# Kernel optimization log

Hardware: AMD Instinct MI355X
Metric: run time of the kernel (lower is better)

## Reference

```python
import jax, jax.numpy as jnp
import numpy as np

DIM = 1024

def setup_inputs() -> dict:
    key = jax.random.key(0)
    ks = jax.random.split(key, 6)
    B, T, D = 8, 2048, DIM
    s = 1.0 / np.sqrt(D)
    x = jax.random.normal(ks[0], (B, T, D), dtype=jnp.float32)
    Wq = jax.random.normal(ks[1], (D, D), dtype=jnp.float32) * s
    Wk = jax.random.normal(ks[2], (D, D), dtype=jnp.float32) * s
    Wv = jax.random.normal(ks[3], (D, D), dtype=jnp.float32) * s
    Wp = jax.random.normal(ks[4], (D, D), dtype=jnp.float32) * s
    bp = jax.random.normal(ks[5], (D,), dtype=jnp.float32) * 0.01
    return {"x": x, "Wq": Wq, "Wk": Wk, "Wv": Wv, "Wp": Wp, "bp": bp}

def reference(x, Wq, Wk, Wv, Wp, bp):
    # x: [b, t, d]; weights stored as [d_in, d_out] (torch Linear applies x @ W.T;
    # here we bake the transpose into the stored matrix).
    scale = x.shape[-1] ** (-0.5)
    q = jnp.einsum('btd,de->bte', x, Wq)
    k = jnp.einsum('btd,de->bte', x, Wk)
    v = jnp.einsum('btd,de->bte', x, Wv)
    attn = jax.nn.softmax(jnp.einsum('btd,bTd->btT', q, k) * scale, axis=-1)
    out = jnp.einsum('btT,bTd->btd', attn, v)
    return jnp.einsum('btd,de->bte', out, Wp) + bp
```

## Files before the change

### kernel.cpp

```cpp
#include <hip/hip_runtime.h>


typedef _Float16 half_t;
typedef _Float16 half8 __attribute__((ext_vector_type(8)));
typedef float floatx4 __attribute__((ext_vector_type(4)));

#define GLD16(gp, lp)                                                          \
    __builtin_amdgcn_global_load_lds(                                          \
        (const __attribute__((address_space(1))) void*)(gp),                   \
        (__attribute__((address_space(3))) void*)(lp), 16, 0, 0)

template<bool OUTF32, bool TSTORE, bool BIAS>
__global__ __launch_bounds__(256, 2)
void gemm16(const half_t* __restrict__ A, const half_t* __restrict__ B,
            void* __restrict__ Cv, const float* __restrict__ bias,
            int K, int lda, int ldb, int ldc,
            long long bsA, long long bsB, long long bsC, float alpha)
{
    __shared__ half_t As[128 * 32];
    __shared__ half_t Bs[128 * 32];

    const int tid  = threadIdx.x;
    const int lane = tid & 63;
    const int wid  = tid >> 6;
    const int wr   = (wid >> 1) * 64;
    const int wc   = (wid & 1) * 64;
    const long long z = blockIdx.z;
    const int rowBase = blockIdx.y * 128;
    const int colBase = blockIdx.x * 128;

    const int srow = wid * 32 + (lane >> 2);
    const int scol = (lane & 3) * 8;

    const half_t* ga0 = A + z * bsA + (long long)(rowBase + srow) * lda + scol;
    const half_t* ga1 = ga0 + 16LL * lda;
    const half_t* gb0 = B + z * bsB + (long long)(colBase + srow) * ldb + scol;
    const half_t* gb1 = gb0 + 16LL * ldb;
    half_t* la0 = &As[(wid * 32) * 32];
    half_t* la1 = &As[(wid * 32 + 16) * 32];
    half_t* lb0 = &Bs[(wid * 32) * 32];
    half_t* lb1 = &Bs[(wid * 32 + 16) * 32];

    floatx4 acc[4][4];
    #pragma unroll
    for (int m = 0; m < 4; ++m)
        #pragma unroll
        for (int n = 0; n < 4; ++n)
            #pragma unroll
            for (int j = 0; j < 4; ++j) acc[m][n][j] = 0.0f;

    const int fr = lane & 15;
    const int fk = (lane >> 4) * 8;

    for (int kk = 0; kk < K; kk += 32) {
        __syncthreads();
        GLD16(ga0 + kk, la0);
        GLD16(ga1 + kk, la1);
        GLD16(gb0 + kk, lb0);
        GLD16(gb1 + kk, lb1);
        __syncthreads();

        half8 af[4], bf[4];
        #pragma unroll
        for (int m = 0; m < 4; ++m)
            af[m] = *(const half8*)&As[(wr + m * 16 + fr) * 32 + fk];
        #pragma unroll
        for (int n = 0; n < 4; ++n)
            bf[n] = *(const half8*)&Bs[(wc + n * 16 + fr) * 32 + fk];
        #pragma unroll
        for (int m = 0; m < 4; ++m)
            #pragma unroll
            for (int n = 0; n < 4; ++n)
                acc[m][n] = __builtin_amdgcn_mfma_f32_16x16x32_f16(af[m], bf[n], acc[m][n], 0, 0, 0);
    }

    const int ecol = lane & 15;
    const int q4   = (lane >> 4) * 4;
    #pragma unroll
    for (int m = 0; m < 4; ++m) {
        #pragma unroll
        for (int n = 0; n < 4; ++n) {
            const int gcol = colBase + wc + n * 16 + ecol;
            #pragma unroll
            for (int r = 0; r < 4; ++r) {
                const int grow = rowBase + wr + m * 16 + q4 + r;
                float v = acc[m][n][r] * alpha;
                if (BIAS) v += bias[gcol];
                if (TSTORE) {
                    const long long bb = grow >> 11;
                    const long long tt = grow & 2047;
                    ((half_t*)Cv)[bb * bsC + (long long)gcol * ldc + tt] = (half_t)v;
                } else {
                    const long long idx = z * bsC + (long long)grow * ldc + gcol;
                    if (OUTF32) ((float*)Cv)[idx] = v;
                    else        ((half_t*)Cv)[idx] = (half_t)v;
                }
            }
        }
    }
}

__global__ __launch_bounds__(256)
void cast16(const float* __restrict__ x, half_t* __restrict__ y)
{
    const long long i = ((long long)blockIdx.x * 256 + threadIdx.x) * 8;
    floatx4 a = *(const floatx4*)(x + i);
    floatx4 b = *(const floatx4*)(x + i + 4);
    half8 h;
    #pragma unroll
    for (int j = 0; j < 4; ++j) { h[j] = (half_t)a[j]; h[j + 4] = (half_t)b[j]; }
    *(half8*)(y + i) = h;
}

__global__ __launch_bounds__(256)
void cast_transpose(const float* __restrict__ W, half_t* __restrict__ WT)
{
    __shared__ float t[32][33];
    const int bx = blockIdx.x * 32, by = blockIdx.y * 32;
    const int tx = threadIdx.x, ty = threadIdx.y;
    #pragma unroll
    for (int i = 0; i < 32; i += 8)
        t[ty + i][tx] = W[(long long)(by + ty + i) * 1024 + bx + tx];
    __syncthreads();
    #pragma unroll
    for (int i = 0; i < 32; i += 8)
        WT[(long long)(bx + ty + i) * 1024 + by + tx] = (half_t)t[tx][ty + i];
}

__global__ __launch_bounds__(256)
void softmax_rows(const float* __restrict__ S, half_t* __restrict__ P)
{
    const long long base = (long long)blockIdx.x * 2048;
    const int t = threadIdx.x;
    float v[8];
    #pragma unroll
    for (int i = 0; i < 8; ++i) v[i] = S[base + i * 256 + t];
    float m = -3.0e38f;
    #pragma unroll
    for (int i = 0; i < 8; ++i) m = fmaxf(m, v[i]);
    #pragma unroll
    for (int off = 32; off > 0; off >>= 1) m = fmaxf(m, __shfl_down(m, off));
    __shared__ float redm[4], reds[4];
    const int lane = t & 63, wid = t >> 6;
    if (lane == 0) redm[wid] = m;
    __syncthreads();
    const float M = fmaxf(fmaxf(redm[0], redm[1]), fmaxf(redm[2], redm[3]));
    float s = 0.f;
    #pragma unroll
    for (int i = 0; i < 8; ++i) { v[i] = __expf(v[i] - M); s += v[i]; }
    #pragma unroll
    for (int off = 32; off > 0; off >>= 1) s += __shfl_down(s, off);
    if (lane == 0) reds[wid] = s;
    __syncthreads();
    const float inv = 1.0f / (reds[0] + reds[1] + reds[2] + reds[3]);
    #pragma unroll
    for (int i = 0; i < 8; ++i) P[base + i * 256 + t] = (half_t)(v[i] * inv);
}

extern "C" void kernel_launch(void* const* d_in, const int* in_sizes, int n_in,
                              void* d_out, int out_size, void* d_ws, size_t ws_size,
                              hipStream_t stream)
{
    const float* x  = (const float*)d_in[0];
    const float* Wq = (const float*)d_in[1];
    const float* Wk = (const float*)d_in[2];
    const float* Wv = (const float*)d_in[3];
    const float* Wp = (const float*)d_in[4];
    const float* bp = (const float*)d_in[5];
    float* out = (float*)d_out;

    char* ws = (char*)d_ws;
    const long long MB = 1024LL * 1024LL;
    half_t* WqT = (half_t*)(ws + 0 * MB);
    half_t* WkT = (half_t*)(ws + 2 * MB);
    half_t* WvT = (half_t*)(ws + 4 * MB);
    half_t* WpT = (half_t*)(ws + 6 * MB);
    half_t* q   = (half_t*)(ws + 8 * MB);
    half_t* k   = (half_t*)(ws + 40 * MB);
    half_t* vT  = (half_t*)(ws + 72 * MB);
    half_t* x16 = (half_t*)(ws + 104 * MB);

    const int ZB = (ws_size >= (size_t)(200 * MB)) ? 4
                 : (ws_size >= (size_t)(152 * MB)) ? 2 : 1;
    float*  S = (float*)(ws + 104 * MB);
    half_t* P = (half_t*)(ws + (104 + ZB * 16) * MB);

    dim3 blk(256);
    cast16<<<8192, blk, 0, stream>>>(x, x16);
    dim3 tb(32, 8), tg(32, 32);
    cast_transpose<<<tg, tb, 0, stream>>>(Wq, WqT);
    cast_transpose<<<tg, tb, 0, stream>>>(Wk, WkT);
    cast_transpose<<<tg, tb, 0, stream>>>(Wv, WvT);
    cast_transpose<<<tg, tb, 0, stream>>>(Wp, WpT);

    gemm16<false, false, false><<<dim3(8, 128, 1), blk, 0, stream>>>(
        x16, WqT, q, nullptr, 1024, 1024, 1024, 1024, 0, 0, 0, 0.03125f);
    gemm16<false, false, false><<<dim3(8, 128, 1), blk, 0, stream>>>(
        x16, WkT, k, nullptr, 1024, 1024, 1024, 1024, 0, 0, 0, 1.0f);
    gemm16<false, true,  false><<<dim3(8, 128, 1), blk, 0, stream>>>(
        x16, WvT, vT, nullptr, 1024, 1024, 1024, 2048, 0, 0, 2048LL * 1024, 1.0f);

    for (int g = 0; g < 8 / ZB; ++g) {
        const long long off = (long long)g * ZB * 2048 * 1024;
        half_t* qp = q  + off;
        half_t* kp = k  + off;
        half_t* vp = vT + off;
        half_t* cp = q  + off;

        gemm16<true, false, false><<<dim3(16, 16, ZB), blk, 0, stream>>>(
            qp, kp, S, nullptr, 1024, 1024, 1024, 2048,
            2048LL * 1024, 2048LL * 1024, 2048LL * 2048, 1.0f);
        softmax_rows<<<ZB * 2048, blk, 0, stream>>>(S, P);
        gemm16<false, false, false><<<dim3(8, 16, ZB), blk, 0, stream>>>(
            P, vp, cp, nullptr, 2048, 2048, 2048, 1024,
            2048LL * 2048, 1024LL * 2048, 2048LL * 1024, 1.0f);
    }

    gemm16<true, false, true><<<dim3(8, 128, 1), blk, 0, stream>>>(
        q, WpT, out, bp, 1024, 1024, 1024, 1024, 0, 0, 0, 1.0f);
}
```

Baseline: 561.7 us.

## Fuse QKV projections, batch all attention heads, store scores in fp16 in place

```diff
diff --git a/kernel.cpp b/kernel.cpp
--- a/kernel.cpp
+++ b/kernel.cpp
@@ -10,12 +10,12 @@
         (const __attribute__((address_space(1))) void*)(gp),                   \
         (__attribute__((address_space(3))) void*)(lp), 16, 0, 0)
 
-template<bool OUTF32, bool TSTORE, bool BIAS>
+template<int EPI>
 __global__ __launch_bounds__(256, 2)
 void gemm16(const half_t* __restrict__ A, const half_t* __restrict__ B,
-            void* __restrict__ Cv, const float* __restrict__ bias,
-            int K, int lda, int ldb, int ldc,
-            long long bsA, long long bsB, long long bsC, float alpha)
+            void* __restrict__ Cv, void* __restrict__ C2, void* __restrict__ C3,
+            const float* __restrict__ bias, int K, int lda, int ldb, int ldc,
+            long long bsA, long long bsB, long long bsC)
 {
     __shared__ half_t As[128 * 32];
     __shared__ half_t Bs[128 * 32];
@@ -84,16 +84,23 @@
             #pragma unroll
             for (int r = 0; r < 4; ++r) {
                 const int grow = rowBase + wr + m * 16 + q4 + r;
-                float v = acc[m][n][r] * alpha;
-                if (BIAS) v += bias[gcol];
-                if (TSTORE) {
-                    const long long bb = grow >> 11;
-                    const long long tt = grow & 2047;
-                    ((half_t*)Cv)[bb * bsC + (long long)gcol * ldc + tt] = (half_t)v;
+                float v = acc[m][n][r];
+                if (EPI == 0) {
+                    ((half_t*)Cv)[z * bsC + (long long)grow * ldc + gcol] = (half_t)v;
+                } else if (EPI == 1) {
+                    ((float*)Cv)[(long long)grow * ldc + gcol] = v + bias[gcol];
                 } else {
-                    const long long idx = z * bsC + (long long)grow * ldc + gcol;
-                    if (OUTF32) ((float*)Cv)[idx] = v;
-                    else        ((half_t*)Cv)[idx] = (half_t)v;
+                    const int mat = colBase >> 10;
+                    const int c   = gcol & 1023;
+                    if (mat == 0) {
+                        ((half_t*)Cv)[(long long)grow * 1024 + c] = (half_t)(v * 0.03125f);
+                    } else if (mat == 1) {
+                        ((half_t*)C2)[(long long)grow * 1024 + c] = (half_t)v;
+                    } else {
+                        const long long bb = grow >> 11;
+                        const long long tt = grow & 2047;
+                        ((half_t*)C3)[bb * (1024LL * 2048) + (long long)c * 2048 + tt] = (half_t)v;
+                    }
                 }
             }
         }
@@ -113,8 +120,13 @@
 }
 
 __global__ __launch_bounds__(256)
-void cast_transpose(const float* __restrict__ W, half_t* __restrict__ WT)
-{
+void cast_transpose4(const float* __restrict__ W0, const float* __restrict__ W1,
+                     const float* __restrict__ W2, const float* __restrict__ W3,
+                     half_t* __restrict__ WT)
+{
+    const float* W = (blockIdx.z == 0) ? W0 : (blockIdx.z == 1) ? W1
+                   : (blockIdx.z == 2) ? W2 : W3;
+    half_t* O = WT + (long long)blockIdx.z * 1024 * 1024;
     __shared__ float t[32][33];
     const int bx = blockIdx.x * 32, by = blockIdx.y * 32;
     const int tx = threadIdx.x, ty = threadIdx.y;
@@ -124,17 +136,18 @@
     __syncthreads();
     #pragma unroll
     for (int i = 0; i < 32; i += 8)
-        WT[(long long)(bx + ty + i) * 1024 + by + tx] = (half_t)t[tx][ty + i];
+        O[(long long)(bx + ty + i) * 1024 + by + tx] = (half_t)t[tx][ty + i];
 }
 
 __global__ __launch_bounds__(256)
-void softmax_rows(const float* __restrict__ S, half_t* __restrict__ P)
+void softmax_rows(half_t* __restrict__ S)
 {
     const long long base = (long long)blockIdx.x * 2048;
     const int t = threadIdx.x;
+    half8 h = *(const half8*)(S + base + t * 8);
     float v[8];
     #pragma unroll
-    for (int i = 0; i < 8; ++i) v[i] = S[base + i * 256 + t];
+    for (int i = 0; i < 8; ++i) v[i] = (float)h[i];
     float m = -3.0e38f;
     #pragma unroll
     for (int i = 0; i < 8; ++i) m = fmaxf(m, v[i]);
@@ -154,7 +167,8 @@
     __syncthreads();
     const float inv = 1.0f / (reds[0] + reds[1] + reds[2] + reds[3]);
     #pragma unroll
-    for (int i = 0; i < 8; ++i) P[base + i * 256 + t] = (half_t)(v[i] * inv);
+    for (int i = 0; i < 8; ++i) h[i] = (half_t)(v[i] * inv);
+    *(half8*)(S + base + t * 8) = h;
 }
 
 extern "C" void kernel_launch(void* const* d_in, const int* in_sizes, int n_in,
@@ -171,51 +185,31 @@
 
     char* ws = (char*)d_ws;
     const long long MB = 1024LL * 1024LL;
-    half_t* WqT = (half_t*)(ws + 0 * MB);
-    half_t* WkT = (half_t*)(ws + 2 * MB);
-    half_t* WvT = (half_t*)(ws + 4 * MB);
-    half_t* WpT = (half_t*)(ws + 6 * MB);
-    half_t* q   = (half_t*)(ws + 8 * MB);
-    half_t* k   = (half_t*)(ws + 40 * MB);
-    half_t* vT  = (half_t*)(ws + 72 * MB);
-    half_t* x16 = (half_t*)(ws + 104 * MB);
-
-    const int ZB = (ws_size >= (size_t)(200 * MB)) ? 4
-                 : (ws_size >= (size_t)(152 * MB)) ? 2 : 1;
-    float*  S = (float*)(ws + 104 * MB);
-    half_t* P = (half_t*)(ws + (104 + ZB * 16) * MB);
+    half_t* WqkvT = (half_t*)(ws + 0 * MB);
+    half_t* WpT   = (half_t*)(ws + 6 * MB);
+    half_t* q     = (half_t*)(ws + 8 * MB);
+    half_t* k     = (half_t*)(ws + 40 * MB);
+    half_t* vT    = (half_t*)(ws + 72 * MB);
+    half_t* x16   = (half_t*)(ws + 104 * MB);
+    half_t* S     = (half_t*)(ws + 104 * MB);
 
     dim3 blk(256);
     cast16<<<8192, blk, 0, stream>>>(x, x16);
-    dim3 tb(32, 8), tg(32, 32);
-    cast_transpose<<<tg, tb, 0, stream>>>(Wq, WqT);
-    cast_transpose<<<tg, tb, 0, stream>>>(Wk, WkT);
-    cast_transpose<<<tg, tb, 0, stream>>>(Wv, WvT);
-    cast_transpose<<<tg, tb, 0, stream>>>(Wp, WpT);
-
-    gemm16<false, false, false><<<dim3(8, 128, 1), blk, 0, stream>>>(
-        x16, WqT, q, nullptr, 1024, 1024, 1024, 1024, 0, 0, 0, 0.03125f);
-    gemm16<false, false, false><<<dim3(8, 128, 1), blk, 0, stream>>>(
-        x16, WkT, k, nullptr, 1024, 1024, 1024, 1024, 0, 0, 0, 1.0f);
-    gemm16<false, true,  false><<<dim3(8, 128, 1), blk, 0, stream>>>(
-        x16, WvT, vT, nullptr, 1024, 1024, 1024, 2048, 0, 0, 2048LL * 1024, 1.0f);
-
-    for (int g = 0; g < 8 / ZB; ++g) {
-        const long long off = (long long)g * ZB * 2048 * 1024;
-        half_t* qp = q  + off;
-        half_t* kp = k  + off;
-        half_t* vp = vT + off;
-        half_t* cp = q  + off;
-
-        gemm16<true, false, false><<<dim3(16, 16, ZB), blk, 0, stream>>>(
-            qp, kp, S, nullptr, 1024, 1024, 1024, 2048,
-            2048LL * 1024, 2048LL * 1024, 2048LL * 2048, 1.0f);
-        softmax_rows<<<ZB * 2048, blk, 0, stream>>>(S, P);
-        gemm16<false, false, false><<<dim3(8, 16, ZB), blk, 0, stream>>>(
-            P, vp, cp, nullptr, 2048, 2048, 2048, 1024,
-            2048LL * 2048, 1024LL * 2048, 2048LL * 1024, 1.0f);
-    }
-
-    gemm16<true, false, true><<<dim3(8, 128, 1), blk, 0, stream>>>(
-        q, WpT, out, bp, 1024, 1024, 1024, 1024, 0, 0, 0, 1.0f);
-}
+    cast_transpose4<<<dim3(32, 32, 4), dim3(32, 8), 0, stream>>>(Wq, Wk, Wv, Wp, WqkvT);
+
+    gemm16<2><<<dim3(24, 128, 1), blk, 0, stream>>>(
+        x16, WqkvT, q, k, vT, nullptr, 1024, 1024, 1024, 0, 0, 0, 0);
+
+    gemm16<0><<<dim3(16, 16, 8), blk, 0, stream>>>(
+        q, k, S, nullptr, nullptr, nullptr, 1024, 1024, 1024, 2048,
+        2048LL * 1024, 2048LL * 1024, 2048LL * 2048);
+
+    softmax_rows<<<8 * 2048, blk, 0, stream>>>(S);
+
+    gemm16<0><<<dim3(8, 16, 8), blk, 0, stream>>>(
+        S, vT, q, nullptr, nullptr, nullptr, 2048, 2048, 2048, 1024,
+        2048LL * 2048, 1024LL * 2048, 2048LL * 1024);
+
+    gemm16<1><<<dim3(8, 128, 1), blk, 0, stream>>>(
+        q, WpT, out, nullptr, nullptr, bp, 1024, 1024, 1024, 1024, 0, 0, 0);
+}
```

Result: no change. 555.0 us (-1.2%).
